# Kernel optimization log

Hardware: AMD Instinct MI355X
Metric: run time of the kernel (lower is better)

The kernel has to match this reference:

```python
import jax, jax.numpy as jnp
import numpy as np

B, G, GI = 128, 360, 174          # batch, n_groups, voxels per group
EF, ET, U = 512, 512, 512         # feat embed, text embed, LSTM units
AU, VOC, T = 32, 5000, 20         # attention units, vocab, max_len


def _leaky(x):
    return jnp.where(x >= 0, x, 0.2 * x)


def _ln(x, g, b, eps=1e-5):
    m = x.mean(-1, keepdims=True)
    v = ((x - m) ** 2).mean(-1, keepdims=True)
    return (x - m) / jnp.sqrt(v + eps) * g + b


def setup_inputs() -> dict:
    key = jax.random.key(0)
    ks = jax.random.split(key, 24)
    def n(k, shape, s=0.02):
        return jax.random.normal(k, shape, jnp.float32) * s
    return {
        "features": jax.random.normal(ks[0], (B, G * GI), jnp.float32),
        "text": jax.random.randint(ks[1], (B, T), 0, VOC),
        "a0": jnp.zeros((B, U), jnp.float32),
        "c0": jnp.zeros((B, U), jnp.float32),
        "enc_W": n(ks[2], (G, GI, EF)), "enc_b": n(ks[3], (G, EF)),
        "enc_ln_g": jnp.ones((EF,), jnp.float32), "enc_ln_b": jnp.zeros((EF,), jnp.float32),
        "attn_W1": n(ks[4], (EF, AU)), "attn_b1": n(ks[5], (AU,)),
        "attn_W2": n(ks[6], (U, AU)), "attn_b2": n(ks[7], (AU,)),
        "attn_V": n(ks[8], (AU, 1)), "attn_bV": n(ks[9], (1,)),
        "emb": n(ks[10], (VOC, ET)),
        "W_ih": n(ks[11], (4 * U, EF + ET)), "W_hh": n(ks[12], (4 * U, U)),
        "b_ih": n(ks[13], (4 * U,)), "b_hh": n(ks[14], (4 * U,)),
        "ln_g": jnp.ones((U,), jnp.float32), "ln_b": jnp.zeros((U,), jnp.float32),
        "dec_W1": n(ks[15], (U, 256)), "dec_b1": n(ks[16], (256,)),
        "dec_W2": n(ks[17], (256, VOC)), "dec_b2": n(ks[18], (VOC,)),
        "subject": 0,
    }


def reference(features, text, a0, c0, enc_W, enc_b, enc_ln_g, enc_ln_b,
              attn_W1, attn_b1, attn_W2, attn_b2, attn_V, attn_bV, emb,
              W_ih, W_hh, b_ih, b_hh, ln_g, ln_b,
              dec_W1, dec_b1, dec_W2, dec_b2, subject):
    # LocallyConnected encoder (weights for the selected subject): groups are
    # 360 contiguous equal splits of the voxel axis -> gather == reshape.
    x = features.reshape(B, G, GI)
    feat = _ln(_leaky(jnp.einsum('bgi,gio->bgo', x, enc_W) + enc_b),
               enc_ln_g, enc_ln_b)                       # [B, G, EF]
    # hidden-independent half of attention, hoisted out of the recurrence
    f1 = jax.nn.relu(jnp.einsum('bge,eu->bgu', feat, attn_W1) + attn_b1)  # [B,G,AU]
    txt = emb[text]                                      # [B, T, ET]

    def step(carry, x_t):
        a, c = carry                                     # [B,U], [B,U]
        h2 = jax.nn.relu(a @ attn_W2 + attn_b2)          # [B, AU]
        score = jnp.tanh(f1 + h2[:, None, :]) @ attn_V + attn_bV  # [B,G,1]
        w = jax.nn.softmax(score, axis=1)
        ctx = jnp.sum(w * feat, axis=1)                  # [B, EF]
        xin = jnp.concatenate([ctx, x_t], axis=1)        # [B, EF+ET]
        gates = xin @ W_ih.T + a @ W_hh.T + b_ih + b_hh  # [B, 4U]
        i, f, g, o = jnp.split(gates, 4, axis=1)         # torch gate order i,f,g,o
        c = jax.nn.sigmoid(f) * c + jax.nn.sigmoid(i) * jnp.tanh(g)
        h = jax.nn.sigmoid(o) * jnp.tanh(c)
        a = _ln(_leaky(h), ln_g, ln_b)                   # fed back as LSTM hidden
        out = jax.nn.softmax(_leaky(a @ dec_W1 + dec_b1) @ dec_W2 + dec_b2, axis=-1)
        return (a, c), (out, w)

    _, (outs, ws) = jax.lax.scan(step, (a0, c0), jnp.swapaxes(txt, 0, 1))
    output = jnp.swapaxes(outs, 0, 1)                    # [B, T, VOC]
    attention_scores = jnp.swapaxes(ws, 0, 1)            # [B, T, G, 1]
    return output, attention_scores
```

## Files before the change

kernel.cpp:

```cpp
#include <hip/hip_runtime.h>
#include <stdint.h>

#define B_  128
#define G_  360
#define GI_ 174
#define EF_ 512
#define U_  512
#define AU_ 32
#define VOC_ 5000
#define T_  20

typedef short short8 __attribute__((ext_vector_type(8)));
typedef float floatx4 __attribute__((ext_vector_type(4)));

#define GLD16(gp, lp) __builtin_amdgcn_global_load_lds( \
    (const __attribute__((address_space(1))) void*)(gp), \
    (__attribute__((address_space(3))) void*)(lp), 16, 0, 0)

__device__ __forceinline__ unsigned short f2bf(float f){
  unsigned u = __float_as_uint(f);
  u += 0x7fffu + ((u>>16)&1u);
  return (unsigned short)(u>>16);
}
__device__ __forceinline__ float2 bfpair(unsigned u){
  float2 r; r.x = __uint_as_float(u<<16); r.y = __uint_as_float(u & 0xffff0000u); return r;
}
__device__ __forceinline__ unsigned packbf(float a, float b){
  return ((unsigned)f2bf(b)<<16) | (unsigned)f2bf(a);
}
__device__ __forceinline__ float sigmf(float x){ return 1.0f/(1.0f + __expf(-x)); }
__device__ __forceinline__ float tanhf_(float x){ return 1.0f - 2.0f/(1.0f + __expf(2.0f*x)); }
__device__ __forceinline__ float leaky_(float x){ return x >= 0.f ? x : 0.2f*x; }

__global__ __launch_bounds__(256) void k_cvt(
    const int* __restrict__ text, const float* __restrict__ emb,
    const float* __restrict__ Wih, const float* __restrict__ Whh,
    const float* __restrict__ bih, const float* __restrict__ bhh,
    const float* __restrict__ W1, const float* __restrict__ b1,
    const float* __restrict__ encg, const float* __restrict__ encb,
    const float* __restrict__ dW1, const float* __restrict__ dW2,
    float* __restrict__ stats, unsigned short* __restrict__ Wstep,
    float* __restrict__ bias_sum, unsigned short* __restrict__ ASbuf,
    unsigned short* __restrict__ W1g, float* __restrict__ f1c,
    unsigned short* __restrict__ dW1t, unsigned short* __restrict__ dW2t)
{
  __shared__ float tile[64][65];
  const int blk = blockIdx.x, tid = threadIdx.x;
  if (blk < 90){
    int i = blk*1024 + tid*4;
    *(float4*)&stats[i] = make_float4(0.f,0.f,0.f,0.f);
  } else if (blk < 2138){
    int j = blk - 90;
    #pragma unroll
    for (int q=0;q<6;++q){
      int c = q*256 + tid;
      float v;
      if (c < 512)       v = Wih[(size_t)j*1024 + 512 + c];
      else if (c < 1024) v = Wih[(size_t)j*1024 + (c - 512)];
      else               v = Whh[(size_t)j*512 + (c - 1024)];
      Wstep[(size_t)j*1536 + c] = f2bf(v);
    }
  } else if (blk < 2146){
    int i = (blk-2138)*256 + tid;
    bias_sum[i] = bih[i] + bhh[i];
  } else if (blk < 4706){
    int r = blk - 2146; int t = r >> 7, b = r & 127;
    int idx = text[b*T_ + t];
    float2 v = *(const float2*)&emb[(size_t)idx*512 + 2*tid];
    ((unsigned*)ASbuf)[(((size_t)r*1536)>>1) + tid] = packbf(v.x, v.y);
  } else if (blk == 4706){
    if (tid < 32){
      float gw = 0.f, bw = 0.f;
      for (int k=0;k<512;++k){
        float wv = W1[(size_t)k*32 + tid];
        float gk = encg[k], bk = encb[k];
        W1g[(size_t)tid*512 + k] = f2bf(gk*wv);
        gw += gk*wv; bw += bk*wv;
      }
      f1c[tid] = gw; f1c[32+tid] = bw + b1[tid];
    }
  } else if (blk < 4739){
    int q = blk - 4707; int kt = q >> 2, nt = q & 3;
    int k0 = kt*64, n0 = nt*64;
    #pragma unroll
    for (int it=0; it<16; ++it){
      int idx = it*256 + tid; int kk = idx>>6, nn = idx&63;
      tile[kk][nn] = dW1[(size_t)(k0+kk)*256 + n0+nn];
    }
    __syncthreads();
    #pragma unroll
    for (int it=0; it<16; ++it){
      int idx = it*256 + tid; int nn = idx>>6, kk = idx&63;
      dW1t[(size_t)(n0+nn)*512 + k0+kk] = f2bf(tile[kk][nn]);
    }
  } else {
    int q = blk - 4739; int kt = q/80, nt = q - kt*80;
    int k0 = kt*64, n0 = nt*64;
    #pragma unroll
    for (int it=0; it<16; ++it){
      int idx = it*256 + tid; int kk = idx>>6, nn = idx&63;
      tile[kk][nn] = (n0+nn < VOC_) ? dW2[(size_t)(k0+kk)*VOC_ + n0+nn] : 0.f;
    }
    __syncthreads();
    #pragma unroll
    for (int it=0; it<16; ++it){
      int idx = it*256 + tid; int nn = idx>>6, kk = idx&63;
      dW2t[(size_t)(n0+nn)*256 + k0+kk] = f2bf(tile[kk][nn]);
    }
  }
}

__device__ __forceinline__ int swz64(int row, int k){
  return row*64 + ((((k>>3) ^ (row&7)))<<3) + (k&7);
}
__global__ __launch_bounds__(256) void k_enc(
    const float* __restrict__ features, const float* __restrict__ encW,
    const float* __restrict__ encB,
    unsigned short* __restrict__ ybuf, float* __restrict__ stats)
{
  __shared__ __align__(16) unsigned short As[128*64];
  __shared__ __align__(16) unsigned short Bs[128*64];
  const int g = blockIdx.y, n0 = blockIdx.x*128;
  const int tid = threadIdx.x, w = tid>>6, l = tid&63;
  const int quad = l>>4, col16 = l&15;
  const int m0w = (w>>1)*64, n0w = (w&1)*64;

  floatx4 acc[4][4];
  #pragma unroll
  for (int mi=0;mi<4;++mi)
    #pragma unroll
    for (int ni=0;ni<4;++ni)
      acc[mi][ni] = (floatx4){0.f,0.f,0.f,0.f};

  for (int c=0; c<3; ++c){
    if (c > 0) __syncthreads();
    #pragma unroll
    for (int q=0; q<8; ++q){
      int idx = q*256 + tid;
      int row = idx >> 4;
      int kq  = idx & 15;
      int kl  = kq*4;
      int kgl = c*64 + kl;
      const float* fp = features + (size_t)row*(G_*GI_) + (size_t)g*GI_ + kgl;
      float4 v;
      if (kgl + 3 < GI_){
        v = *(const float4*)fp;
      } else {
        v.x = (kgl+0 < GI_) ? fp[0] : 0.f;
        v.y = (kgl+1 < GI_) ? fp[1] : 0.f;
        v.z = (kgl+2 < GI_) ? fp[2] : 0.f;
        v.w = (kgl+3 < GI_) ? fp[3] : 0.f;
      }
      int e = row*64 + (((kl>>3) ^ (row&7))<<3) + (kl&7);
      uint2 pk; pk.x = packbf(v.x, v.y); pk.y = packbf(v.z, v.w);
      *(uint2*)&As[e] = pk;
    }
    #pragma unroll
    for (int z=0; z<16; ++z){
      int kk = w + 4*z;
      int k  = c*64 + kk;
      if (k < GI_){
        const float* wp = encW + ((size_t)g*GI_ + k)*512 + n0;
        float2 v = *(const float2*)&wp[2*l];
        Bs[swz64(2*l,   kk)] = f2bf(v.x);
        Bs[swz64(2*l+1, kk)] = f2bf(v.y);
      } else {
        Bs[swz64(2*l,   kk)] = 0;
        Bs[swz64(2*l+1, kk)] = 0;
      }
    }
    __syncthreads();
    #pragma unroll
    for (int it=0; it<2; ++it){
      int kk = it*32 + quad*8;
      short8 af[4], bfr[4];
      #pragma unroll
      for (int mi=0;mi<4;++mi){
        int row = m0w + mi*16 + col16;
        af[mi] = *(const short8*)&As[row*64 + (((kk>>3) ^ (row&7))<<3)];
      }
      #pragma unroll
      for (int ni=0;ni<4;++ni){
        int rowb = n0w + ni*16 + col16;
        bfr[ni] = *(const short8*)&Bs[rowb*64 + (((kk>>3) ^ (rowb&7))<<3)];
      }
      #pragma unroll
      for (int mi=0;mi<4;++mi)
        #pragma unroll
        for (int ni=0;ni<4;++ni)
          acc[mi][ni] = __builtin_amdgcn_mfma_f32_16x16x32_bf16(af[mi], bfr[ni], acc[mi][ni], 0,0,0);
    }
  }

  #pragma unroll
  for (int mi=0;mi<4;++mi){
    float sy[4] = {0.f,0.f,0.f,0.f};
    float sq[4] = {0.f,0.f,0.f,0.f};
    #pragma unroll
    for (int ni=0;ni<4;++ni){
      int nG = n0 + n0w + ni*16 + col16;
      float bv = encB[(size_t)g*512 + nG];
      #pragma unroll
      for (int reg=0;reg<4;++reg){
        int row = m0w + mi*16 + quad*4 + reg;
        float y = leaky_(acc[mi][ni][reg] + bv);
        unsigned short yh = f2bf(y);
        ybuf[((size_t)row*G_ + g)*512 + nG] = yh;
        float yr = __uint_as_float(((unsigned)yh)<<16);
        sy[reg] += yr; sq[reg] += yr*yr;
      }
    }
    #pragma unroll
    for (int reg=0; reg<4; ++reg){
      float a = sy[reg], bq = sq[reg];
      #pragma unroll
      for (int mk=1; mk<16; mk<<=1){ a += __shfl_xor(a, mk, 64); bq += __shfl_xor(bq, mk, 64); }
      if (col16 == 0){
        int row = m0w + mi*16 + quad*4 + reg;
        atomicAdd(&stats[((size_t)row*G_ + g)*2],     a);
        atomicAdd(&stats[((size_t)row*G_ + g)*2 + 1], bq);
      }
    }
  }
}

template<int TN, int NBK, int MODE, int KSPLIT=1>
__global__ __launch_bounds__(256) void k_gemm(
    const unsigned short* __restrict__ A, int lda,
    const unsigned short* __restrict__ Bt, int ldb,
    const float* __restrict__ bias,
    float* __restrict__ outf, unsigned short* __restrict__ outh,
    const float* __restrict__ stats, float* __restrict__ stats2,
    const float* __restrict__ f1c)
{
  constexpr int NI = TN/32;
  __shared__ __align__(16) unsigned short As[128*64];
  __shared__ __align__(16) unsigned short Bs[TN*64];
  const int tid = threadIdx.x;
  const int w = tid >> 6, l = tid & 63;
  const int n0 = blockIdx.x * TN;
  const int ks = (KSPLIT > 1) ? blockIdx.y : 0;
  const int r0 = (KSPLIT > 1) ? 0 : blockIdx.y * 128;
  const int quad = l>>4, col16 = l&15;
  const int m0w = (w>>1)*64, n0w = (w&1)*(TN/2);
  const int arow = w*32, brow = w*(TN/4);

  const unsigned short* Ag = A + (size_t)(r0 + arow + (l>>3))*lda + (l&7)*8;
  const unsigned short* Bg = Bt + (size_t)(n0 + brow + (l>>3))*ldb + (l&7)*8;

  floatx4 acc[4][NI];
  #pragma unroll
  for (int mi=0;mi<4;++mi)
    #pragma unroll
    for (int ni=0;ni<NI;++ni)
      acc[mi][ni] = (floatx4){0.f,0.f,0.f,0.f};

  for (int it=0; it<NBK; ++it){
    int k0 = (ks*NBK + it)*64;
    #pragma unroll
    for (int q=0;q<4;++q)
      GLD16(Ag + (size_t)q*8*lda + k0, As + (arow + q*8)*64);
    #pragma unroll
    for (int q=0;q<TN/32;++q)
      GLD16(Bg + (size_t)q*8*ldb + k0, Bs + (brow + q*8)*64);
    __syncthreads();
    #pragma unroll
    for (int kc=0;kc<2;++kc){
      int koff = kc*32 + quad*8;
      short8 af[4], bfr[NI];
      #pragma unroll
      for (int mi=0;mi<4;++mi)
        af[mi] = *(const short8*)&As[(m0w + mi*16 + col16)*64 + koff];
      #pragma unroll
      for (int ni=0;ni<NI;++ni)
        bfr[ni] = *(const short8*)&Bs[(n0w + ni*16 + col16)*64 + koff];
      #pragma unroll
      for (int mi=0;mi<4;++mi)
        #pragma unroll
        for (int ni=0;ni<NI;++ni)
          acc[mi][ni] = __builtin_amdgcn_mfma_f32_16x16x32_bf16(af[mi], bfr[ni], acc[mi][ni], 0,0,0);
    }
    __syncthreads();
  }

  if constexpr (MODE == 0){
    float* op = outf + (size_t)ks*(128*2048);
    #pragma unroll
    for (int ni=0; ni<NI; ++ni){
      int nG = n0 + n0w + ni*16 + col16;
      float bv = (KSPLIT == 1 || ks == 0) ? bias[nG] : 0.f;
      #pragma unroll
      for (int mi=0; mi<4; ++mi)
        #pragma unroll
        for (int reg=0; reg<4; ++reg){
          int r = r0 + m0w + mi*16 + quad*4 + reg;
          op[(size_t)r*2048 + nG] = acc[mi][ni][reg] + bv;
        }
    }
  } else if constexpr (MODE == 1){
    int nG = n0w + col16;
    float gw = f1c[nG], bwv = f1c[32+nG];
    #pragma unroll
    for (int mi=0; mi<4; ++mi)
      #pragma unroll
      for (int reg=0; reg<4; ++reg){
        int r = r0 + m0w + mi*16 + quad*4 + reg;
        float2 st = *(const float2*)&stats[(size_t)r*2];
        float m = st.x * (1.f/512.f);
        float var = st.y * (1.f/512.f) - m*m;
        float rs = rsqrtf(var + 1e-5f);
        float v = rs*(acc[mi][0][reg] - m*gw) + bwv;
        v = v > 0.f ? v : 0.f;
        outf[(size_t)r*32 + nG] = v;
        if (((w&1)==0) && col16==0){
          stats2[(size_t)r*2] = m; stats2[(size_t)r*2+1] = rs;
        }
      }
  } else if constexpr (MODE == 2){
    #pragma unroll
    for (int ni=0; ni<NI; ++ni){
      int nG = n0 + n0w + ni*16 + col16;
      float bv = bias[nG];
      #pragma unroll
      for (int mi=0; mi<4; ++mi)
        #pragma unroll
        for (int reg=0; reg<4; ++reg){
          int r = r0 + m0w + mi*16 + quad*4 + reg;
          outh[(size_t)r*256 + nG] = f2bf(leaky_(acc[mi][ni][reg] + bv));
        }
    }
  } else {
    #pragma unroll
    for (int ni=0; ni<NI; ++ni){
      int nG = n0 + n0w + ni*16 + col16;
      if (nG < VOC_){
        float bv = bias[nG];
        #pragma unroll
        for (int mi=0; mi<4; ++mi)
          #pragma unroll
          for (int reg=0; reg<4; ++reg){
            int r = r0 + m0w + mi*16 + quad*4 + reg;
            int bb = r & 127, tt = r >> 7;
            outf[((size_t)bb*T_ + tt)*VOC_ + nG] = acc[mi][ni][reg] + bv;
          }
      }
    }
  }
}

__global__ __launch_bounds__(256) void k_cellattn(
    const float* __restrict__ gall, const float* __restrict__ c_in,
    float* __restrict__ c_out, const float* __restrict__ a0,
    const float* __restrict__ lng, const float* __restrict__ lnb,
    const float* __restrict__ W2, const float* __restrict__ b2,
    const float* __restrict__ Vv, const float* __restrict__ bV,
    const float* __restrict__ f1, const unsigned short* __restrict__ ybuf,
    const float* __restrict__ stats2,
    const float* __restrict__ encg, const float* __restrict__ encb,
    unsigned short* __restrict__ ASlot, unsigned short* __restrict__ a_bf,
    float* __restrict__ att_out, int t_att, int mode_cell, int do_attn)
{
  __shared__ float a_s[512];
  __shared__ float sc[G_];
  __shared__ float hred[8*32];
  __shared__ float h2s[32];
  __shared__ float red[16];
  __shared__ float mrs[2];
  const int b = blockIdx.x, tid = threadIdx.x;
  const int wv = tid >> 6, ln = tid & 63;

  if (mode_cell){
    float hl2[2];
    #pragma unroll
    for (int q=0;q<2;++q){
      int u = tid + q*256;
      size_t base = (size_t)b*2048;
      float gi = 0.f, gf = 0.f, gc = 0.f, go = 0.f;
      #pragma unroll
      for (int s=0;s<4;++s){
        const float* gp = gall + (size_t)s*(128*2048) + base;
        gi += gp[u]; gf += gp[512+u]; gc += gp[1024+u]; go += gp[1536+u];
      }
      float c = sigmf(gf)*c_in[(size_t)b*512+u] + sigmf(gi)*tanhf_(gc);
      c_out[(size_t)b*512+u] = c;
      hl2[q] = leaky_(sigmf(go)*tanhf_(c));
    }
    float s = hl2[0]+hl2[1], ss = hl2[0]*hl2[0]+hl2[1]*hl2[1];
    #pragma unroll
    for (int mk=1;mk<64;mk<<=1){ s += __shfl_xor(s,mk,64); ss += __shfl_xor(ss,mk,64); }
    if (ln==0){ red[wv]=s; red[8+wv]=ss; }
    __syncthreads();
    if (tid==0){
      float S  = red[0]+red[1]+red[2]+red[3];
      float SS = red[8]+red[9]+red[10]+red[11];
      float mean = S*(1.f/512.f);
      float var  = SS*(1.f/512.f) - mean*mean;
      mrs[0]=mean; mrs[1]=rsqrtf(var+1e-5f);
    }
    __syncthreads();
    float mean = mrs[0], rstd = mrs[1];
    #pragma unroll
    for (int q=0;q<2;++q){
      int u = tid + q*256;
      float av = (hl2[q]-mean)*rstd*lng[u] + lnb[u];
      a_s[u] = av;
      a_bf[(size_t)b*512 + u] = f2bf(av);
      if (do_attn) ASlot[(size_t)b*1536 + 1024 + u] = f2bf(av);
    }
  } else {
    #pragma unroll
    for (int q=0;q<2;++q){
      int u = tid + q*256;
      float av = a0[(size_t)b*512 + u];
      a_s[u] = av;
      ASlot[(size_t)b*1536 + 1024 + u] = f2bf(av);
    }
  }
  __syncthreads();
  if (!do_attn) return;

  {
    int u = tid & 31, ch = tid >> 5;
    float p = 0.f;
    const float* w2p = W2 + (size_t)ch*64*32 + u;
    const float* ap = a_s + ch*64;
    #pragma unroll 8
    for (int e=0;e<64;++e) p += ap[e]*w2p[(size_t)e*32];
    hred[ch*32+u] = p;
  }
  __syncthreads();
  if (tid < 32){
    float p = hred[tid];
    #pragma unroll
    for (int ch=1; ch<8; ++ch) p += hred[ch*32+tid];
    p += b2[tid];
    h2s[tid] = p>0.f? p:0.f;
  }
  __syncthreads();
  float bVv = bV[0];
  for (int gg = tid; gg < G_; gg += 256){
    const float* fp = f1 + ((size_t)b*G_ + gg)*32;
    float s = bVv;
    #pragma unroll
    for (int u=0;u<32;++u) s += tanhf_(fp[u] + h2s[u]) * Vv[u];
    sc[gg] = s;
  }
  __syncthreads();
  float mx = -1e30f;
  for (int gg=tid; gg<G_; gg+=256) mx = fmaxf(mx, sc[gg]);
  #pragma unroll
  for (int mk=1;mk<64;mk<<=1) mx = fmaxf(mx, __shfl_xor(mx,mk,64));
  if (ln==0) red[wv]=mx;
  __syncthreads();
  if (tid==0) red[0] = fmaxf(fmaxf(red[0],red[1]),fmaxf(red[2],red[3]));
  __syncthreads();
  mx = red[0];
  float psum = 0.f;
  for (int gg=tid; gg<G_; gg+=256){
    float e = __expf(sc[gg]-mx);
    sc[gg] = e; psum += e;
  }
  #pragma unroll
  for (int mk=1;mk<64;mk<<=1) psum += __shfl_xor(psum,mk,64);
  if (ln==0) red[8+wv]=psum;
  __syncthreads();
  if (tid==0) red[8] = red[8]+red[9]+red[10]+red[11];
  __syncthreads();
  float inv = 1.f/red[8];
  float Mop = 0.f;
  float* wout = att_out + ((size_t)b*T_ + t_att)*G_;
  for (int gg=tid; gg<G_; gg+=256){
    float wg = sc[gg]*inv;
    wout[gg] = wg;
    float2 st = *(const float2*)&stats2[((size_t)b*G_+gg)*2];
    sc[gg] = wg*st.y;
    Mop += wg*st.x*st.y;
  }
  #pragma unroll
  for (int mk=1;mk<64;mk<<=1) Mop += __shfl_xor(Mop,mk,64);
  if (ln==0) red[4+wv] = Mop;
  __syncthreads();
  if (tid==0) mrs[0] = red[4]+red[5]+red[6]+red[7];
  __syncthreads();
  float Mo = mrs[0];
  {
    const unsigned* fp = (const unsigned*)ybuf + ((size_t)b*G_)*256 + tid;
    float c0v=0.f, c1v=0.f;
    for (int gg=0; gg<G_; ++gg){
      float2 p = bfpair(fp[(size_t)gg*256]);
      float wq = sc[gg];
      c0v += wq*p.x; c1v += wq*p.y;
    }
    int e0 = 2*tid;
    float ctx0 = encg[e0]  *(c0v - Mo) + encb[e0];
    float ctx1 = encg[e0+1]*(c1v - Mo) + encb[e0+1];
    ((unsigned*)ASlot)[(((size_t)b*1536 + 512)>>1) + tid] = packbf(ctx0, ctx1);
  }
}

__global__ __launch_bounds__(256) void k_softmax(float* __restrict__ outp)
{
  __shared__ float red[8];
  const size_t row = (size_t)blockIdx.x * VOC_;
  const int tid = threadIdx.x;
  const int wv = tid >> 6, ln = tid & 63;
  float v[20];
  float mx = -1e30f;
  #pragma unroll
  for (int k=0;k<20;++k){
    int idx = tid + k*256;
    v[k] = (idx < VOC_) ? outp[row+idx] : -1e30f;
    mx = fmaxf(mx, v[k]);
  }
  #pragma unroll
  for (int mk=1;mk<64;mk<<=1) mx = fmaxf(mx,__shfl_xor(mx,mk,64));
  if (ln==0) red[wv] = mx;
  __syncthreads();
  if (tid==0) red[0]=fmaxf(fmaxf(red[0],red[1]),fmaxf(red[2],red[3]));
  __syncthreads();
  mx = red[0];
  float s=0.f;
  #pragma unroll
  for (int k=0;k<20;++k){ v[k] = __expf(v[k]-mx); s += v[k]; }
  #pragma unroll
  for (int mk=1;mk<64;mk<<=1) s += __shfl_xor(s,mk,64);
  if (ln==0) red[4+wv]=s;
  __syncthreads();
  if (tid==0) red[4]=red[4]+red[5]+red[6]+red[7];
  __syncthreads();
  float inv = 1.f/red[4];
  #pragma unroll
  for (int k=0;k<20;++k){
    int idx = tid + k*256;
    if (idx < VOC_) outp[row+idx] = v[k]*inv;
  }
}

extern "C" void kernel_launch(void* const* d_in, const int* in_sizes, int n_in,
                              void* d_out, int out_size, void* d_ws, size_t ws_size,
                              hipStream_t stream) {
  const float* features = (const float*)d_in[0];
  const int*   text     = (const int*)d_in[1];
  const float* a0    = (const float*)d_in[2];
  const float* c0    = (const float*)d_in[3];
  const float* encW  = (const float*)d_in[4];
  const float* encB  = (const float*)d_in[5];
  const float* encLNg= (const float*)d_in[6];
  const float* encLNb= (const float*)d_in[7];
  const float* attnW1= (const float*)d_in[8];
  const float* attnb1= (const float*)d_in[9];
  const float* attnW2= (const float*)d_in[10];
  const float* attnb2= (const float*)d_in[11];
  const float* attnV = (const float*)d_in[12];
  const float* attnbV= (const float*)d_in[13];
  const float* emb   = (const float*)d_in[14];
  const float* Wih   = (const float*)d_in[15];
  const float* Whh   = (const float*)d_in[16];
  const float* bih   = (const float*)d_in[17];
  const float* bhh   = (const float*)d_in[18];
  const float* lng   = (const float*)d_in[19];
  const float* lnb   = (const float*)d_in[20];
  const float* dW1   = (const float*)d_in[21];
  const float* db1   = (const float*)d_in[22];
  const float* dW2   = (const float*)d_in[23];
  const float* db2   = (const float*)d_in[24];

  uint8_t* w8 = (uint8_t*)d_ws;
  unsigned short* ybuf   = (unsigned short*)(w8);
  float*          stats  = (float*)(w8 + 47185920);
  float*          stats2 = (float*)(w8 + 47554560);
  float*          f1b    = (float*)(w8 + 47923200);
  unsigned short* ASbuf  = (unsigned short*)(w8 + 53821440);
  unsigned short* Wstep  = (unsigned short*)(w8 + 61685760);
  float*          bias_sum=(float*)(w8 + 67977216);
  unsigned short* W1g    = (unsigned short*)(w8 + 67985408);
  float*          f1c    = (float*)(w8 + 68018176);
  unsigned short* dW1t   = (unsigned short*)(w8 + 68018432);
  unsigned short* dW2t   = (unsigned short*)(w8 + 68280576);
  float*          gbuf   = (float*)(w8 + 70902016);
  float*          cws    = (float*)(w8 + 71950592);
  unsigned short* a_bf   = (unsigned short*)(w8 + 72212736);
  unsigned short* d1bf   = (unsigned short*)(w8 + 74834176);

  float* outp = (float*)d_out;
  float* att  = outp + 12800000;
  float* gsplit = outp;
  (void)gbuf;

  hipLaunchKernelGGL(k_cvt, dim3(5059), dim3(256), 0, stream,
                     text, emb, Wih, Whh, bih, bhh, attnW1, attnb1,
                     encLNg, encLNb, dW1, dW2,
                     stats, Wstep, bias_sum, ASbuf, W1g, f1c, dW1t, dW2t);
  hipLaunchKernelGGL(k_enc, dim3(4,360), dim3(256), 0, stream,
                     features, encW, encB, ybuf, stats);
  hipLaunchKernelGGL((k_gemm<32,8,1>), dim3(1,360), dim3(256), 0, stream,
                     ybuf, 512, W1g, 512, (const float*)nullptr,
                     f1b, (unsigned short*)nullptr, stats, stats2, f1c);
  hipLaunchKernelGGL(k_cellattn, dim3(128), dim3(256), 0, stream,
                     gsplit, c0, cws, a0, lng, lnb, attnW2, attnb2, attnV, attnbV,
                     f1b, ybuf, stats2, encLNg, encLNb,
                     ASbuf, a_bf, att, 0, 0, 1);
  for (int t=0; t<T_; ++t){
    hipLaunchKernelGGL((k_gemm<64,6,0,4>), dim3(32,4), dim3(256), 0, stream,
                       ASbuf + (size_t)t*128*1536, 1536, Wstep, 1536, bias_sum,
                       gsplit, (unsigned short*)nullptr,
                       (const float*)nullptr, (float*)nullptr, (const float*)nullptr);
    int da = (t < T_-1) ? 1 : 0;
    unsigned short* slot = ASbuf + (size_t)((t+1 < T_) ? (t+1) : 0)*128*1536;
    hipLaunchKernelGGL(k_cellattn, dim3(128), dim3(256), 0, stream,
                       gsplit, (t==0)?c0:cws, cws, a0, lng, lnb,
                       attnW2, attnb2, attnV, attnbV,
                       f1b, ybuf, stats2, encLNg, encLNb,
                       slot, a_bf + (size_t)t*128*512, att, t+1, 1, da);
  }
  hipLaunchKernelGGL((k_gemm<128,8,2>), dim3(2,20), dim3(256), 0, stream,
                     a_bf, 512, dW1t, 512, db1,
                     (float*)nullptr, d1bf, (const float*)nullptr, (float*)nullptr,
                     (const float*)nullptr);
  hipLaunchKernelGGL((k_gemm<128,4,3>), dim3(40,20), dim3(256), 0, stream,
                     d1bf, 256, dW2t, 256, db2,
                     outp, (unsigned short*)nullptr, (const float*)nullptr,
                     (float*)nullptr, (const float*)nullptr);
  hipLaunchKernelGGL(k_softmax, dim3(2560), dim3(256), 0, stream, outp);
}
```

Before: 1.157 ms.

## Hoist text-embedding gate GEMM out of recurrence and add split-K per-step gate kernel

The embedding half of the LSTM input projection (x_t @ W_ih_text) does not depend on the hidden state, so it is now computed for all timesteps in one batched GEMM before the loop. Each step then runs a new split-K MFMA kernel over only the ctx and hidden columns (1024 of K), loading pre-swizzled bf16 tiles directly into LDS, and the cell kernel sums 8 partials plus the precomputed text gates. The weight and activation layouts are XOR-swizzled at write time so the direct-to-LDS loads avoid bank conflicts. It also sets a min-blocks-per-CU launch bound on the encoder and restructures its weight-load loop. The cost is extra partial-sum traffic through the output buffer and one large upfront GEMM.

```diff
diff --git a/kernel.cpp b/kernel.cpp
--- a/kernel.cpp
+++ b/kernel.cpp
@@ -31,6 +31,10 @@
 __device__ __forceinline__ float sigmf(float x){ return 1.0f/(1.0f + __expf(-x)); }
 __device__ __forceinline__ float tanhf_(float x){ return 1.0f - 2.0f/(1.0f + __expf(2.0f*x)); }
 __device__ __forceinline__ float leaky_(float x){ return x >= 0.f ? x : 0.2f*x; }
+
+__device__ __forceinline__ int swzcol(int cc, int e){
+  return (cc & ~63) | ((((cc>>3)&7) ^ e)<<3) | (cc&7);
+}
 
 __global__ __launch_bounds__(256) void k_cvt(
     const int* __restrict__ text, const float* __restrict__ emb,
@@ -58,7 +62,9 @@
       if (c < 512)       v = Wih[(size_t)j*1024 + 512 + c];
       else if (c < 1024) v = Wih[(size_t)j*1024 + (c - 512)];
       else               v = Whh[(size_t)j*512 + (c - 1024)];
-      Wstep[(size_t)j*1536 + c] = f2bf(v);
+      int cd = c;
+      if (c >= 512) cd = 512 + swzcol(c - 512, j&7);
+      Wstep[(size_t)j*1536 + cd] = f2bf(v);
     }
   } else if (blk < 2146){
     int i = (blk-2138)*256 + tid;
@@ -113,7 +119,7 @@
 __device__ __forceinline__ int swz64(int row, int k){
   return row*64 + ((((k>>3) ^ (row&7)))<<3) + (k&7);
 }
-__global__ __launch_bounds__(256) void k_enc(
+__global__ __launch_bounds__(256, 3) void k_enc(
     const float* __restrict__ features, const float* __restrict__ encW,
     const float* __restrict__ encB,
     unsigned short* __restrict__ ybuf, float* __restrict__ stats)
@@ -156,17 +162,21 @@
       *(uint2*)&As[e] = pk;
     }
     #pragma unroll
-    for (int z=0; z<16; ++z){
-      int kk = w + 4*z;
-      int k  = c*64 + kk;
-      if (k < GI_){
-        const float* wp = encW + ((size_t)g*GI_ + k)*512 + n0;
-        float2 v = *(const float2*)&wp[2*l];
-        Bs[swz64(2*l,   kk)] = f2bf(v.x);
-        Bs[swz64(2*l+1, kk)] = f2bf(v.y);
-      } else {
-        Bs[swz64(2*l,   kk)] = 0;
-        Bs[swz64(2*l+1, kk)] = 0;
+    for (int zb=0; zb<2; ++zb){
+      #pragma unroll
+      for (int z=0; z<8; ++z){
+        int zz = zb*8 + z;
+        int kk = w + 4*zz;
+        int k  = c*64 + kk;
+        if (k < GI_){
+          const float* wp = encW + ((size_t)g*GI_ + k)*512 + n0;
+          float2 v = *(const float2*)&wp[2*l];
+          Bs[swz64(2*l,   kk)] = f2bf(v.x);
+          Bs[swz64(2*l+1, kk)] = f2bf(v.y);
+        } else {
+          Bs[swz64(2*l,   kk)] = 0;
+          Bs[swz64(2*l+1, kk)] = 0;
+        }
       }
     }
     __syncthreads();
@@ -348,8 +358,77 @@
   }
 }
 
+__global__ __launch_bounds__(256) void k_gates(
+    const unsigned short* __restrict__ A,
+    const unsigned short* __restrict__ Bt,
+    float* __restrict__ outp)
+{
+  __shared__ __align__(16) unsigned short As[128*128];
+  __shared__ __align__(16) unsigned short Bs[64*128];
+  const int tid = threadIdx.x, w = tid>>6, l = tid&63;
+  const int ks = blockIdx.y;
+  const int n0 = blockIdx.x*64;
+  const int quad = l>>4, col16 = l&15;
+  const int m0w = (w>>1)*64, n0w = (w&1)*32;
+  const int arow = w*32, brow = w*16;
+
+  const unsigned short* Ag = A + (size_t)(arow + (l>>4))*1536 + ks*128 + (l&15)*8;
+  const unsigned short* Bg = Bt + (size_t)(n0 + brow + (l>>4))*1536 + 512 + ks*128 + (l&15)*8;
+  #pragma unroll
+  for (int q=0;q<8;++q)
+    GLD16(Ag + (size_t)q*4*1536, As + (arow + q*4)*128);
+  #pragma unroll
+  for (int q=0;q<4;++q)
+    GLD16(Bg + (size_t)q*4*1536, Bs + (brow + q*4)*128);
+
+  floatx4 acc[4][2];
+  #pragma unroll
+  for (int mi=0;mi<4;++mi)
+    #pragma unroll
+    for (int ni=0;ni<2;++ni)
+      acc[mi][ni] = (floatx4){0.f,0.f,0.f,0.f};
+
+  __syncthreads();
+  #pragma unroll
+  for (int kc=0;kc<4;++kc){
+    int koff = kc*32 + quad*8;
+    int kbase = koff & 64;
+    int kx = (koff>>3)&7;
+    short8 af[4], bfr[2];
+    #pragma unroll
+    for (int mi=0;mi<4;++mi){
+      int row = m0w + mi*16 + col16;
+      af[mi] = *(const short8*)&As[row*128 + kbase + ((kx ^ (row&7))<<3)];
+    }
+    #pragma unroll
+    for (int ni=0;ni<2;++ni){
+      int rowb = n0w + ni*16 + col16;
+      bfr[ni] = *(const short8*)&Bs[rowb*128 + kbase + ((kx ^ (rowb&7))<<3)];
+    }
+    #pragma unroll
+    for (int mi=0;mi<4;++mi)
+      #pragma unroll
+      for (int ni=0;ni<2;++ni)
+        acc[mi][ni] = __builtin_amdgcn_mfma_f32_16x16x32_bf16(af[mi], bfr[ni], acc[mi][ni], 0,0,0);
+  }
+
+  float* op = outp + (size_t)ks*(128*2048);
+  #pragma unroll
+  for (int ni=0; ni<2; ++ni){
+    int nG = n0 + n0w + ni*16 + col16;
+    #pragma unroll
+    for (int mi=0; mi<4; ++mi)
+      #pragma unroll
+      for (int reg=0; reg<4; ++reg){
+        int r = m0w + mi*16 + quad*4 + reg;
+        op[(size_t)r*2048 + nG] = acc[mi][ni][reg];
+      }
+  }
+}
+
 __global__ __launch_bounds__(256) void k_cellattn(
-    const float* __restrict__ gall, const float* __restrict__ c_in,
+    const float* __restrict__ gall, const float* __restrict__ gtx,
+    const float* __restrict__ c_in,
     float* __restrict__ c_out, const float* __restrict__ a0,
     const float* __restrict__ lng, const float* __restrict__ lnb,
     const float* __restrict__ W2, const float* __restrict__ b2,
@@ -375,9 +454,12 @@
     for (int q=0;q<2;++q){
       int u = tid + q*256;
       size_t base = (size_t)b*2048;
-      float gi = 0.f, gf = 0.f, gc = 0.f, go = 0.f;
-      #pragma unroll
-      for (int s=0;s<4;++s){
+      float gi = gtx[base+u];
+      float gf = gtx[base+512+u];
+      float gc = gtx[base+1024+u];
+      float go = gtx[base+1536+u];
+      #pragma unroll
+      for (int s=0;s<8;++s){
         const float* gp = gall + (size_t)s*(128*2048) + base;
         gi += gp[u]; gf += gp[512+u]; gc += gp[1024+u]; go += gp[1536+u];
       }
@@ -405,7 +487,10 @@
       float av = (hl2[q]-mean)*rstd*lng[u] + lnb[u];
       a_s[u] = av;
       a_bf[(size_t)b*512 + u] = f2bf(av);
-      if (do_attn) ASlot[(size_t)b*1536 + 1024 + u] = f2bf(av);
+      if (do_attn){
+        int pc = swzcol(512 + u, b&7);
+        ASlot[(size_t)b*1536 + 512 + pc] = f2bf(av);
+      }
     }
   } else {
     #pragma unroll
@@ -413,7 +498,8 @@
       int u = tid + q*256;
       float av = a0[(size_t)b*512 + u];
       a_s[u] = av;
-      ASlot[(size_t)b*1536 + 1024 + u] = f2bf(av);
+      int pc = swzcol(512 + u, b&7);
+      ASlot[(size_t)b*1536 + 512 + pc] = f2bf(av);
     }
   }
   __syncthreads();
@@ -494,7 +580,8 @@
     int e0 = 2*tid;
     float ctx0 = encg[e0]  *(c0v - Mo) + encb[e0];
     float ctx1 = encg[e0+1]*(c1v - Mo) + encb[e0+1];
-    ((unsigned*)ASlot)[(((size_t)b*1536 + 512)>>1) + tid] = packbf(ctx0, ctx1);
+    int pc = swzcol(2*tid, b&7);
+    ((unsigned*)ASlot)[((size_t)b*1536 + 512 + pc)>>1] = packbf(ctx0, ctx1);
   }
 }
 
@@ -577,7 +664,6 @@
   float*          f1c    = (float*)(w8 + 68018176);
   unsigned short* dW1t   = (unsigned short*)(w8 + 68018432);
   unsigned short* dW2t   = (unsigned short*)(w8 + 68280576);
-  float*          gbuf   = (float*)(w8 + 70902016);
   float*          cws    = (float*)(w8 + 71950592);
   unsigned short* a_bf   = (unsigned short*)(w8 + 72212736);
   unsigned short* d1bf   = (unsigned short*)(w8 + 74834176);
@@ -585,7 +671,7 @@
   float* outp = (float*)d_out;
   float* att  = outp + 12800000;
   float* gsplit = outp;
-  (void)gbuf;
+  float* gtxt   = outp + 8*128*2048;
 
   hipLaunchKernelGGL(k_cvt, dim3(5059), dim3(256), 0, stream,
                      text, emb, Wih, Whh, bih, bhh, attnW1, attnb1,
@@ -593,22 +679,24 @@
                      stats, Wstep, bias_sum, ASbuf, W1g, f1c, dW1t, dW2t);
   hipLaunchKernelGGL(k_enc, dim3(4,360), dim3(256), 0, stream,
                      features, encW, encB, ybuf, stats);
+  hipLaunchKernelGGL((k_gemm<64,8,0>), dim3(32,20), dim3(256), 0, stream,
+                     ASbuf, 1536, Wstep, 1536, bias_sum,
+                     gtxt, (unsigned short*)nullptr,
+                     (const float*)nullptr, (float*)nullptr, (const float*)nullptr);
   hipLaunchKernelGGL((k_gemm<32,8,1>), dim3(1,360), dim3(256), 0, stream,
                      ybuf, 512, W1g, 512, (const float*)nullptr,
                      f1b, (unsigned short*)nullptr, stats, stats2, f1c);
   hipLaunchKernelGGL(k_cellattn, dim3(128), dim3(256), 0, stream,
-                     gsplit, c0, cws, a0, lng, lnb, attnW2, attnb2, attnV, attnbV,
+                     gsplit, gtxt, c0, cws, a0, lng, lnb, attnW2, attnb2, attnV, attnbV,
                      f1b, ybuf, stats2, encLNg, encLNb,
                      ASbuf, a_bf, att, 0, 0, 1);
   for (int t=0; t<T_; ++t){
-    hipLaunchKernelGGL((k_gemm<64,6,0,4>), dim3(32,4), dim3(256), 0, stream,
-                       ASbuf + (size_t)t*128*1536, 1536, Wstep, 1536, bias_sum,
-                       gsplit, (unsigned short*)nullptr,
-                       (const float*)nullptr, (float*)nullptr, (const float*)nullptr);
+    hipLaunchKernelGGL(k_gates, dim3(32,8), dim3(256), 0, stream,
+                       ASbuf + (size_t)t*128*1536 + 512, Wstep, gsplit);
     int da = (t < T_-1) ? 1 : 0;
     unsigned short* slot = ASbuf + (size_t)((t+1 < T_) ? (t+1) : 0)*128*1536;
     hipLaunchKernelGGL(k_cellattn, dim3(128), dim3(256), 0, stream,
-                       gsplit, (t==0)?c0:cws, cws, a0, lng, lnb,
+                       gsplit, gtxt + (size_t)t*128*2048, (t==0)?c0:cws, cws, a0, lng, lnb,
                        attnW2, attnb2, attnV, attnbV,
                        f1b, ybuf, stats2, encLNg, encLNb,
                        slot, a_bf + (size_t)t*128*512, att, t+1, 1, da);
```

Result: no change. 1.170 ms (+1.1%).
